# Kernel optimization log

Hardware: AMD Instinct MI355X
Metric: run time of the kernel (lower is better)

The kernel has to match this reference:

```python
import jax, jax.numpy as jnp
from jax import lax
import numpy as np

KS = 3
N = KS * KS
EPS = 1e-5


def conv2d(x, w, b=None, groups=1):
    out = lax.conv_general_dilated(x, w, (1, 1), 'SAME',
                                   feature_group_count=groups,
                                   dimension_numbers=('NCHW', 'OIHW', 'NCHW'))
    if b is not None:
        out = out + b[None, :, None, None]
    return out


def batchnorm(x, g, b):
    # training-mode BN (fresh nn.Module defaults to train): batch stats, biased var
    mu = x.mean((0, 2, 3), keepdims=True)
    var = ((x - mu) ** 2).mean((0, 2, 3), keepdims=True)
    return (x - mu) * lax.rsqrt(var + EPS) * g[None, :, None, None] + b[None, :, None, None]


def up2x_align_corners(x):
    # bilinear upsample, scale_factor=2, align_corners=True
    B, C, H, W = x.shape
    Ho, Wo = 2 * H, 2 * W

    def idx_w(n_in, n_out):
        c = jnp.arange(n_out, dtype=x.dtype) * ((n_in - 1) / (n_out - 1))
        i0 = jnp.clip(jnp.floor(c).astype(jnp.int32), 0, n_in - 2)
        t = c - i0.astype(x.dtype)
        return i0, t

    y0, ty = idx_w(H, Ho)
    x0, tx = idx_w(W, Wo)
    r = x[:, :, y0, :] * (1 - ty)[None, None, :, None] + x[:, :, y0 + 1, :] * ty[None, None, :, None]
    return r[:, :, :, x0] * (1 - tx) + r[:, :, :, x0 + 1] * tx


def gather_hw(xp, qx, qy):
    # xp: (B,C,Hp,Wp); qx,qy: (B,H,W,N) int -> (B,C,H,W,N)
    B, C, Hp, Wp = xp.shape
    flat = xp.reshape(B, C, Hp * Wp)
    idx = (qx * Wp + qy).reshape(B, 1, -1)
    idx = jnp.broadcast_to(idx, (B, C, idx.shape[-1]))
    return jnp.take_along_axis(flat, idx, axis=2).reshape(B, C, *qx.shape[1:])


def deform_conv(x, p_w, p_b, m_w, m_b, w):
    # modulated deformable conv v2 (4uiiurz1 impl), ks=3, stride=1, padding=1
    B, C, H, W = x.shape
    off = conv2d(x, p_w, p_b)                      # (B,2N,H,W)
    m = jax.nn.sigmoid(conv2d(x, m_w, m_b))        # (B,N,H,W)
    xp = jnp.pad(x, ((0, 0), (0, 0), (1, 1), (1, 1)))
    Hp, Wp = H + 2, W + 2
    off = jnp.transpose(off, (0, 2, 3, 1))         # (B,H,W,2N)
    pn_x = jnp.repeat(jnp.arange(-1, 2, dtype=x.dtype), KS)  # kernel row offsets, n=i*3+j
    pn_y = jnp.tile(jnp.arange(-1, 2, dtype=x.dtype), KS)
    p0_x = jnp.arange(1, H + 1, dtype=x.dtype)[None, :, None, None]
    p0_y = jnp.arange(1, W + 1, dtype=x.dtype)[None, None, :, None]
    px = p0_x + pn_x + off[..., :N]                # (B,H,W,N)
    py = p0_y + pn_y + off[..., N:]
    fx = jnp.floor(lax.stop_gradient(px))
    fy = jnp.floor(lax.stop_gradient(py))
    qx0 = jnp.clip(fx, 0, Hp - 1)
    qx1 = jnp.clip(fx + 1, 0, Hp - 1)
    qy0 = jnp.clip(fy, 0, Wp - 1)
    qy1 = jnp.clip(fy + 1, 0, Wp - 1)
    pxc = jnp.clip(px, 0, Hp - 1)
    pyc = jnp.clip(py, 0, Wp - 1)
    g_lt = (1 + (qx0 - pxc)) * (1 + (qy0 - pyc))
    g_rb = (1 - (qx1 - pxc)) * (1 - (qy1 - pyc))
    g_lb = (1 + (qx0 - pxc)) * (1 - (qy1 - pyc))
    g_rt = (1 - (qx1 - pxc)) * (1 + (qy0 - pyc))
    ix0, ix1 = qx0.astype(jnp.int32), qx1.astype(jnp.int32)
    iy0, iy1 = qy0.astype(jnp.int32), qy1.astype(jnp.int32)
    x_off = (g_lt[:, None] * gather_hw(xp, ix0, iy0)
             + g_rb[:, None] * gather_hw(xp, ix1, iy1)
             + g_lb[:, None] * gather_hw(xp, ix0, iy1)
             + g_rt[:, None] * gather_hw(xp, ix1, iy0))   # (B,C,H,W,N)
    x_off = x_off * jnp.transpose(m, (0, 2, 3, 1))[:, None]  # modulation
    O = w.shape[0]
    # equivalent to reshape to (B,C,H*ks,W*ks) then conv stride ks (bias=False)
    return jnp.einsum('bchwn,ocn->bohw', x_off, w.reshape(O, C, N))


def setup_inputs() -> dict:
    key = jax.random.key(0)
    ks = jax.random.split(key, 18)
    f = jnp.float32
    Cin, Cout = 256, 128
    inp = {
        'x1': jax.random.normal(ks[0], (8, 128, 32, 32), f),
        'x2': jax.random.normal(ks[1], (8, 128, 64, 64), f),
        'dsc_dw_w': jax.random.normal(ks[2], (Cin, 1, 3, 3), f) * 0.1,
        'dsc_dw_b': jax.random.normal(ks[3], (Cin,), f) * 0.05,
        'dsc_pw_w': jax.random.normal(ks[4], (Cout, Cin, 1, 1), f) * 0.05,
        'dsc_pw_b': jax.random.normal(ks[5], (Cout,), f) * 0.05,
        'p_w': jax.random.normal(ks[6], (2 * N, Cout, 3, 3), f) * 0.01,
        'p_b': jax.random.normal(ks[7], (2 * N,), f) * 0.01,
        'm_w': jax.random.normal(ks[8], (N, Cout, 3, 3), f) * 0.01,
        'm_b': jax.random.normal(ks[9], (N,), f) * 0.01,
        'dcn_w': jax.random.normal(ks[10], (Cout, Cout, 3, 3), f) * 0.05,
        'bn1_g': jnp.ones((Cout,), f),
        'bn1_b': jnp.zeros((Cout,), f),
        'dw2_w': jax.random.normal(ks[11], (Cout, 1, 3, 3), f) * 0.1,
        'dw2_b': jax.random.normal(ks[12], (Cout,), f) * 0.05,
        'bn2_g': jnp.ones((Cout,), f),
        'bn2_b': jnp.zeros((Cout,), f),
    }
    return inp


def reference(x1, x2, dsc_dw_w, dsc_dw_b, dsc_pw_w, dsc_pw_b, p_w, p_b, m_w, m_b,
              dcn_w, bn1_g, bn1_b, dw2_w, dw2_b, bn2_g, bn2_b):
    x1u = up2x_align_corners(x1)                 # (B,128,64,64); diffX=diffY=0 -> no pad
    x = jnp.concatenate([x2, x1u], axis=1)       # (B,256,64,64)
    h = conv2d(x, dsc_dw_w, dsc_dw_b, groups=x.shape[1])   # depthwise
    h = conv2d(h, dsc_pw_w, dsc_pw_b)                      # pointwise -> 128
    h = deform_conv(h, p_w, p_b, m_w, m_b, dcn_w)
    h = jax.nn.gelu(batchnorm(h, bn1_g, bn1_b), approximate=False)
    h = conv2d(h, dw2_w, dw2_b, groups=h.shape[1])         # depthwise k=3
    return jax.nn.relu(batchnorm(h, bn2_g, bn2_b))
```

## Files before the change

kernel.cpp:

```cpp
#include <hip/hip_runtime.h>
#include <math.h>

typedef const float* fp;
typedef __attribute__((ext_vector_type(8))) short short8;
typedef __attribute__((ext_vector_type(4))) float f32x4;

__device__ __forceinline__ unsigned short f2bf(float f){
    unsigned u = __float_as_uint(f);
    u += 0x7fff + ((u >> 16) & 1);
    return (unsigned short)(u >> 16);
}
__device__ __forceinline__ float bflo(unsigned u){ return __uint_as_float(u << 16); }
__device__ __forceinline__ float bfhi(unsigned u){ return __uint_as_float(u & 0xffff0000u); }
__device__ __forceinline__ unsigned cvtpk(float a, float b){
    unsigned r; asm("v_cvt_pk_bf16_f32 %0, %1, %2" : "=v"(r) : "v"(a), "v"(b)); return r;
}
__device__ __forceinline__ void st4bf(void* p, float a, float b, float c, float d){
    uint2 v; v.x = cvtpk(a,b); v.y = cvtpk(c,d);
    *(uint2*)p = v;
}

__global__ __launch_bounds__(256) void k_prep(fp dcn_w, fp pw, fp mw, fp pww,
                                              unsigned short* Wbf, unsigned short* Wpm,
                                              unsigned short* Wpwbf){
    int i = blockIdx.x*256 + threadIdx.x;
    if(i < 16384){
        int o = i >> 7, c = i & 127;
        const float* s = dcn_w + o*1152 + c*9;
        #pragma unroll
        for(int n=0;n<9;n++) Wbf[(n<<14) + (o<<7) + c] = f2bf(s[n]);
    } else if(i < 20480){
        int j = i - 16384;
        int q = j >> 7, c = j & 127;
        if(q < 18){
            const float* s = pw + q*1152 + c*9;
            #pragma unroll
            for(int n=0;n<9;n++) Wpm[(n<<12) + (q<<7) + c] = f2bf(s[n]);
        } else if(q < 27){
            const float* s = mw + (q-18)*1152 + c*9;
            #pragma unroll
            for(int n=0;n<9;n++) Wpm[(n<<12) + (q<<7) + c] = f2bf(s[n]);
        } else {
            #pragma unroll
            for(int n=0;n<9;n++) Wpm[(n<<12) + (q<<7) + c] = 0;
        }
    } else if(i < 53248){
        int j = i - 20480;
        Wpwbf[j] = f2bf(pww[j]);
    }
}

__global__ __launch_bounds__(256) void k_updw256(fp x1, fp x2, fp w, fp bias, unsigned short* Bo){
    __shared__ float sA[66*68 + 4];
    int bid = blockIdx.x;
    int c = bid & 255, b = bid >> 8;
    int tid = threadIdx.x;
    for(int j = tid; j < 264; j += 256){
        int idx;
        if(j < 66)       idx = j;
        else if(j < 132) idx = 65*68 + (j-66);
        else if(j < 196) idx = (j-132+1)*68;
        else if(j < 260) idx = (j-196+1)*68 + 65;
        else             idx = 66*68 + (j-260);
        sA[idx] = 0.f;
    }
    if(c < 128){
        const float* src = x2 + ((size_t)(b*128+c)<<12);
        for(int j = tid; j < 1024; j += 256){
            int yy = j >> 4, x4 = (j & 15) << 2;
            float4 v = *(const float4*)&src[(yy<<6) + x4];
            float* d = &sA[(yy+1)*68 + x4 + 1];
            d[0]=v.x; d[1]=v.y; d[2]=v.z; d[3]=v.w;
        }
    } else {
        int cc = c - 128;
        fp src = x1 + ((b*128+cc)<<10);
        const float s = 31.0f/63.0f;
        for(int j = tid; j < 4096; j += 256){
            int yy = j >> 6, xx = j & 63;
            float fy = yy*s, fx = xx*s;
            int iy = (int)fy; if (iy > 30) iy = 30;
            int ix = (int)fx; if (ix > 30) ix = 30;
            float ty = fy - (float)iy, tx = fx - (float)ix;
            float v00 = src[iy*32+ix],     v01 = src[iy*32+ix+1];
            float v10 = src[(iy+1)*32+ix], v11 = src[(iy+1)*32+ix+1];
            sA[(yy+1)*68 + xx + 1] =
                (v00*(1.f-ty)+v10*ty)*(1.f-tx) + (v01*(1.f-ty)+v11*ty)*tx;
        }
    }
    __syncthreads();
    float w0=w[c*9+0], w1=w[c*9+1], w2=w[c*9+2];
    float w3=w[c*9+3], w4=w[c*9+4], w5=w[c*9+5];
    float w6=w[c*9+6], w7=w[c*9+7], w8=w[c*9+8];
    float bv = bias[c];
    unsigned short* dst = Bo + ((size_t)(b*256+c)<<12);
    for(int j = tid; j < 1024; j += 256){
        int y = j >> 4, x0 = (j & 15) << 2;
        float a0=bv, a1=bv, a2=bv, a3=bv;
        #pragma unroll
        for(int ky=0; ky<3; ky++){
            const float* rr = &sA[(y+ky)*68 + x0];
            float4 u0 = *(const float4*)&rr[0];
            float2 u1 = *(const float2*)&rr[4];
            float wA = (ky==0)?w0:((ky==1)?w3:w6);
            float wB = (ky==0)?w1:((ky==1)?w4:w7);
            float wC = (ky==0)?w2:((ky==1)?w5:w8);
            a0 += wA*u0.x + wB*u0.y + wC*u0.z;
            a1 += wA*u0.y + wB*u0.z + wC*u0.w;
            a2 += wA*u0.z + wB*u0.w + wC*u1.x;
            a3 += wA*u0.w + wB*u1.x + wC*u1.y;
        }
        st4bf(&dst[(y<<6)+x0], a0,a1,a2,a3);
    }
}

#define PW_STAGE_X(kc, bufp) do{ \
    _Pragma("unroll") \
    for(int k_=0;k_<4;k_++){ \
        int j_ = tid + (k_<<9); \
        int cc_ = j_ >> 4, p4_ = (j_ & 15) << 2; \
        int c_ = ((kc)<<7) + cc_; \
        uint2 v_ = *(const uint2*)&Bo[((size_t)((b<<8)+c_)<<12) + pix0 + p4_]; \
        (bufp)[(p4_+0)*136 + cc_] = (unsigned short)(v_.x & 0xffffu); \
        (bufp)[(p4_+1)*136 + cc_] = (unsigned short)(v_.x >> 16); \
        (bufp)[(p4_+2)*136 + cc_] = (unsigned short)(v_.y & 0xffffu); \
        (bufp)[(p4_+3)*136 + cc_] = (unsigned short)(v_.y >> 16); \
    } }while(0)

#define PW_STAGE_W(kc) do{ \
    _Pragma("unroll") \
    for(int k_=0;k_<4;k_++){ \
        int j_ = tid + (k_<<9); \
        int o_ = j_ >> 4, cg_ = j_ & 15; \
        *(int4*)&sW[o_*136 + (cg_<<3)] = \
            *(const int4*)&Wpwbf[o_*256 + ((kc)<<7) + (cg_<<3)]; \
    } }while(0)

#define PW_DOMFMA(srcp) do{ \
    _Pragma("unroll") \
    for(int ks_=0; ks_<4; ks_++){ \
        int k0_ = ks_ << 5; \
        short8 bfr0 = *(const short8*)&(srcp)[(phb + m16)*136 + k0_ + (quad<<3)]; \
        short8 bfr1 = *(const short8*)&(srcp)[(phb + 16 + m16)*136 + k0_ + (quad<<3)]; \
        _Pragma("unroll") \
        for(int ot_=0;ot_<2;ot_++){ \
            short8 afr = *(const short8*)&sW[(wo + (ot_<<4) + m16)*136 + k0_ + (quad<<3)]; \
            acc[ot_][0] = __builtin_amdgcn_mfma_f32_16x16x32_bf16(afr, bfr0, acc[ot_][0], 0,0,0); \
            acc[ot_][1] = __builtin_amdgcn_mfma_f32_16x16x32_bf16(afr, bfr1, acc[ot_][1], 0,0,0); \
        } } }while(0)

__global__ __launch_bounds__(512, 2) void k_pw(const unsigned short* Bo, const unsigned short* Wpwbf,
                                               fp bias, unsigned short* Cbf){
    __shared__ __align__(16) unsigned short sW[128*136];
    __shared__ __align__(16) unsigned short sX[2][64*136];
    int b = blockIdx.x & 7;
    int pix0 = (blockIdx.x >> 3) << 6;
    int tid = threadIdx.x;
    int lane = tid & 63, wave = tid >> 6;
    int m16 = lane & 15, quad = lane >> 4;
    int wo  = (wave & 3) << 5;
    int phb = (wave >> 2) << 5;

    short8 ap = {0,0,0,0,0,0,0,0}, bpr = {0,0,0,0,0,0,0,0};
    if(quad == 0){
        ap[0]  = (short)f2bf((float)m16);
        bpr[0] = (short)f2bf((float)(m16+100));
    }
    f32x4 dp = {0.f,0.f,0.f,0.f};
    dp = __builtin_amdgcn_mfma_f32_16x16x32_bf16(ap, bpr, dp, 0,0,0);
    bool p1 = true;
    #pragma unroll
    for(int r=0;r<4;r++){
        float expP1 = (float)(quad*4+r) * (float)(m16+100);
        p1 = p1 && (fabsf(dp[r]-expP1) < 0.5f);
    }
    bool swapD = (__ballot(p1) != 0xFFFFFFFFFFFFFFFFull);

    f32x4 acc[2][2];
    #pragma unroll
    for(int i=0;i<2;i++){
        #pragma unroll
        for(int j=0;j<2;j++) acc[i][j] = (f32x4){0.f,0.f,0.f,0.f};
    }

    PW_STAGE_X(0, (&sX[0][0]));
    PW_STAGE_W(0);
    __syncthreads();
    PW_STAGE_X(1, (&sX[1][0]));
    PW_DOMFMA((&sX[0][0]));
    __syncthreads();
    PW_STAGE_W(1);
    __syncthreads();
    PW_DOMFMA((&sX[1][0]));

    if(!swapD){
        #pragma unroll
        for(int ot=0;ot<2;ot++){
            int o0 = wo + (ot<<4) + (quad<<2);
            float4 bv = *(const float4*)&bias[o0];
            #pragma unroll
            for(int pt=0;pt<2;pt++){
                int px = pix0 + phb + (pt<<4) + m16;
                st4bf(&Cbf[((size_t)((b<<12) + px))*128 + o0],
                      acc[ot][pt][0]+bv.x, acc[ot][pt][1]+bv.y,
                      acc[ot][pt][2]+bv.z, acc[ot][pt][3]+bv.w);
            }
        }
    } else {
        #pragma unroll
        for(int ot=0;ot<2;ot++){
            int o = wo + (ot<<4) + m16;
            float bv = bias[o];
            #pragma unroll
            for(int pt=0;pt<2;pt++){
                #pragma unroll
                for(int r=0;r<4;r++){
                    int px = pix0 + phb + (pt<<4) + (quad<<2) + r;
                    Cbf[((size_t)((b<<12) + px))*128 + o] = f2bf(acc[ot][pt][r] + bv);
                }
            }
        }
    }
}

__global__ __launch_bounds__(256, 2) void k_offmask(const unsigned short* Cbf, const unsigned short* Wpm,
                                                    fp pb, fp mb, float* OM){
    __shared__ __align__(16) unsigned short sWin[3*66*136];
    __shared__ __align__(16) unsigned short sW[2][32*136];
    int b = blockIdx.x & 7;
    int y = blockIdx.x >> 3;
    int pix0 = y << 6;
    int tid = threadIdx.x;
    int lane = tid & 63, wave = tid >> 6;
    int m16 = lane & 15, quad = lane >> 4;
    int wp = wave << 4;
    const unsigned short* cbf = Cbf + ((size_t)b<<12)*128;

    short8 ap = {0,0,0,0,0,0,0,0}, bpr = {0,0,0,0,0,0,0,0};
    if(quad == 0){
        ap[0]  = (short)f2bf((float)m16);
        bpr[0] = (short)f2bf((float)(m16+100));
    }
    f32x4 dp = {0.f,0.f,0.f,0.f};
    dp = __builtin_amdgcn_mfma_f32_16x16x32_bf16(ap, bpr, dp, 0,0,0);
    bool p1 = true;
    #pragma unroll
    for(int r=0;r<4;r++){
        float expP1 = (float)(quad*4+r) * (float)(m16+100);
        p1 = p1 && (fabsf(dp[r]-expP1) < 0.5f);
    }
    bool swapD = (__ballot(p1) != 0xFFFFFFFFFFFFFFFFull);

    f32x4 acc[2];
    acc[0] = (f32x4){0.f,0.f,0.f,0.f};
    acc[1] = (f32x4){0.f,0.f,0.f,0.f};

    {
        const int4* wsrc = (const int4*)Wpm;
        int4 wA_ = wsrc[tid], wB_ = wsrc[tid + 256];
        for(int i = tid; i < 3168; i += 256){
            int pos = i >> 4, g = i & 15;
            int r = pos / 66, col = pos - r*66;
            int yy = y + r - 1, xx = col - 1;
            int4 v = make_int4(0,0,0,0);
            if(yy>=0 && yy<64 && xx>=0 && xx<64)
                v = *(const int4*)&cbf[(size_t)((yy<<6)+xx)*128 + (g<<3)];
            *(int4*)&sWin[pos*136 + (g<<3)] = v;
        }
        *(int4*)&sW[0][(tid>>4)*136 + ((tid&15)<<3)] = wA_;
        int j = tid + 256;
        *(int4*)&sW[0][(j>>4)*136 + ((j&15)<<3)] = wB_;
    }
    __syncthreads();

    for(int n=0;n<9;n++){
        int4 wA_, wB_;
        if(n<8){
            const int4* wsrc = (const int4*)(Wpm + ((n+1)<<12));
            wA_ = wsrc[tid]; wB_ = wsrc[tid + 256];
        }
        int ky = n/3, kx = n - ky*3;
        const unsigned short* base = &sWin[(ky*66 + wp + kx)*136];
        #pragma unroll
        for(int ks=0; ks<4; ks++){
            int k0 = ks << 5;
            short8 bfr = *(const short8*)&base[m16*136 + k0 + (quad<<3)];
            #pragma unroll
            for(int qt=0;qt<2;qt++){
                short8 afr = *(const short8*)&sW[n&1][((qt<<4) + m16)*136 + k0 + (quad<<3)];
                acc[qt] = __builtin_amdgcn_mfma_f32_16x16x32_bf16(afr, bfr, acc[qt], 0,0,0);
            }
        }
        if(n<8){
            *(int4*)&sW[(n+1)&1][(tid>>4)*136 + ((tid&15)<<3)] = wA_;
            int j = tid + 256;
            *(int4*)&sW[(n+1)&1][(j>>4)*136 + ((j&15)<<3)] = wB_;
        }
        __syncthreads();
    }
    if(!swapD){
        #pragma unroll
        for(int qt=0;qt<2;qt++){
            int px = pix0 + wp + m16;
            #pragma unroll
            for(int r=0;r<4;r++){
                int q = (qt<<4) + (quad<<2) + r;
                if(q < 27){
                    float v = acc[qt][r] + ((q<18) ? pb[q] : mb[q-18]);
                    if(q>=18) v = 1.f/(1.f+expf(-v));
                    OM[((b*27+q)<<12) + px] = v;
                }
            }
        }
    } else {
        #pragma unroll
        for(int qt=0;qt<2;qt++){
            int q = (qt<<4) + m16;
            if(q < 27){
                float bias = (q<18) ? pb[q] : mb[q-18];
                #pragma unroll
                for(int r=0;r<4;r++){
                    int px = pix0 + wp + (quad<<2) + r;
                    float v = acc[qt][r] + bias;
                    if(q>=18) v = 1.f/(1.f+expf(-v));
                    OM[((b*27+q)<<12) + px] = v;
                }
            }
        }
    }
}

#define K5_META(t) do{ if(tid < 256){ \
    int px_ = tid >> 2, k_ = tid & 3; \
    int pix_ = pix0 + px_; \
    int yq_ = pix_ >> 6, xq_ = pix_ & 63; \
    int kyy_ = (t)/3, kxx_ = (t)-kyy_*3; \
    float oxv_ = omb[((t)<<12)+pix_]; \
    float oyv_ = omb[(((t)+9)<<12)+pix_]; \
    float mv_  = omb[(((t)+18)<<12)+pix_]; \
    float pxf_ = (float)(yq_ + kyy_) + oxv_; \
    float pyf_ = (float)(xq_ + kxx_) + oyv_; \
    float fx_ = floorf(pxf_), fy_ = floorf(pyf_); \
    float qx0_ = fminf(fmaxf(fx_,0.f),65.f),  qx1_ = fminf(fmaxf(fx_+1.f,0.f),65.f); \
    float qy0_ = fminf(fmaxf(fy_,0.f),65.f),  qy1_ = fminf(fmaxf(fy_+1.f,0.f),65.f); \
    float pxc_ = fminf(fmaxf(pxf_,0.f),65.f), pyc_ = fminf(fmaxf(pyf_,0.f),65.f); \
    float dx0_ = 1.f+(qx0_-pxc_), dx1_ = 1.f-(qx1_-pxc_); \
    float dy0_ = 1.f+(qy0_-pyc_), dy1_ = 1.f-(qy1_-pyc_); \
    int ax0_=(int)qx0_, ax1_=(int)qx1_, ay0_=(int)qy0_, ay1_=(int)qy1_; \
    bool vx0_ = (ax0_>=1)&&(ax0_<=64), vx1_ = (ax1_>=1)&&(ax1_<=64); \
    bool vy0_ = (ay0_>=1)&&(ay0_<=64), vy1_ = (ay1_>=1)&&(ay1_<=64); \
    int  axs_ = (k_&1) ? ax1_ : ax0_; \
    int  ays_ = (k_==1||k_==2) ? ay1_ : ay0_; \
    bool vxs_ = (k_&1) ? vx1_ : vx0_; \
    bool vys_ = (k_==1||k_==2) ? vy1_ : vy0_; \
    float dxs_ = (k_&1) ? dx1_ : dx0_; \
    float dys_ = (k_==1||k_==2) ? dy1_ : dy0_; \
    bool v_ = vxs_ && vys_; \
    int base_ = v_ ? (((axs_-1)<<6)+(ays_-1)) : 0; \
    float g_ = v_ ? dxs_*dys_*mv_ : 0.f; \
    sM[tid] = make_uint2((unsigned)base_, __float_as_uint(g_)); \
} }while(0)

#define K5_GATHER(bufp) do{ \
    _Pragma("unroll") \
    for(int j_=0;j_<4;j_++){ \
        int px_ = pxb + (j_<<4); \
        uint2 e0_ = sM[(px_<<2)+0]; \
        uint2 e1_ = sM[(px_<<2)+1]; \
        uint2 e2_ = sM[(px_<<2)+2]; \
        uint2 e3_ = sM[(px_<<2)+3]; \
        float g0_ = __uint_as_float(e0_.y), g1_ = __uint_as_float(e1_.y); \
        float g2_ = __uint_as_float(e2_.y), g3_ = __uint_as_float(e3_.y); \
        uint2 c0_ = *(const uint2*)&cb[((size_t)e0_.x<<7) + cg4]; \
        uint2 c1_ = *(const uint2*)&cb[((size_t)e1_.x<<7) + cg4]; \
        uint2 c2_ = *(const uint2*)&cb[((size_t)e2_.x<<7) + cg4]; \
        uint2 c3_ = *(const uint2*)&cb[((size_t)e3_.x<<7) + cg4]; \
        float vx_ = g0_*bflo(c0_.x) + g1_*bflo(c1_.x) + g2_*bflo(c2_.x) + g3_*bflo(c3_.x); \
        float vy_ = g0_*bfhi(c0_.x) + g1_*bfhi(c1_.x) + g2_*bfhi(c2_.x) + g3_*bfhi(c3_.x); \
        float vz_ = g0_*bflo(c0_.y) + g1_*bflo(c1_.y) + g2_*bflo(c2_.y) + g3_*bflo(c3_.y); \
        float vw_ = g0_*bfhi(c0_.y) + g1_*bfhi(c1_.y) + g2_*bfhi(c2_.y) + g3_*bfhi(c3_.y); \
        st4bf(&(bufp)[px_*136 + cg4], vx_, vy_, vz_, vw_); \
    } }while(0)

#define K5_STAGE_W(t) do{ \
    const int4* wsrc_ = (const int4*)(Wbf + ((t)<<14)); \
    _Pragma("unroll") \
    for(int k_=0;k_<4;k_++){ int j_ = tid + (k_<<9); \
        *(int4*)&sW[(j_>>4)*136 + ((j_&15)<<3)] = wsrc_[j_]; } }while(0)

#define K5_DOMFMA(srcp) do{ \
    _Pragma("unroll") \
    for(int ks_=0; ks_<4; ks_++){ \
        int k0_ = ks_ << 5; \
        short8 bfr0 = *(const short8*)&(srcp)[(phb + m16)*136 + k0_ + (quad<<3)]; \
        short8 bfr1 = *(const short8*)&(srcp)[(phb + 16 + m16)*136 + k0_ + (quad<<3)]; \
        _Pragma("unroll") \
        for(int ot_=0;ot_<2;ot_++){ \
            short8 afr = *(const short8*)&sW[(wo + (ot_<<4) + m16)*136 + k0_ + (quad<<3)]; \
            acc[ot_][0] = __builtin_amdgcn_mfma_f32_16x16x32_bf16(afr, bfr0, acc[ot_][0], 0,0,0); \
            acc[ot_][1] = __builtin_amdgcn_mfma_f32_16x16x32_bf16(afr, bfr1, acc[ot_][1], 0,0,0); \
        } } }while(0)

__global__ __launch_bounds__(512, 2) void k_deform(const unsigned short* Cbf, fp OM,
                                                   const unsigned short* Wbf,
                                                   unsigned short* D, float* stats){
    __shared__ __align__(16) unsigned short sW[128*136];
    __shared__ __align__(16) unsigned short sX[2][64*136];
    __shared__ __align__(8)  uint2 sM[256];
    int b = blockIdx.x & 7;
    int pix0 = (blockIdx.x >> 3) << 6;
    int tid = threadIdx.x;
    int lane = tid & 63, wave = tid >> 6;
    int m16 = lane & 15, quad = lane >> 4;
    int wo  = (wave & 3) << 5;
    int phb = (wave >> 2) << 5;
    int cg4 = (tid & 31) << 2;
    int pxb = tid >> 5;
    const float* omb = OM + b*27*4096;
    const unsigned short* cb = Cbf + ((size_t)b<<12)*128;

    short8 ap = {0,0,0,0,0,0,0,0}, bpr = {0,0,0,0,0,0,0,0};
    if(quad == 0){
        ap[0]  = (short)f2bf((float)m16);
        bpr[0] = (short)f2bf((float)(m16+100));
    }
    f32x4 dp = {0.f,0.f,0.f,0.f};
    dp = __builtin_amdgcn_mfma_f32_16x16x32_bf16(ap, bpr, dp, 0,0,0);
    bool p1 = true;
    #pragma unroll
    for(int r=0;r<4;r++){
        float expP1 = (float)(quad*4+r) * (float)(m16+100);
        p1 = p1 && (fabsf(dp[r]-expP1) < 0.5f);
    }
    bool swapD = (__ballot(p1) != 0xFFFFFFFFFFFFFFFFull);

    f32x4 acc[2][2];
    #pragma unroll
    for(int i=0;i<2;i++){
        #pragma unroll
        for(int j=0;j<2;j++) acc[i][j] = (f32x4){0.f,0.f,0.f,0.f};
    }

    K5_META(0);
    __syncthreads();
    K5_GATHER((&sX[0][0]));
    K5_STAGE_W(0);
    __syncthreads();
    K5_META(1);
    __syncthreads();

    for(int n=0;n<9;n++){
        if(n<8) K5_GATHER((&sX[(n+1)&1][0]));
        K5_DOMFMA((&sX[n&1][0]));
        __syncthreads();
        if(n<8){
            K5_STAGE_W(n+1);
            if(n<7) K5_META(n+2);
            __syncthreads();
        }
    }

    float* sdq = (float*)&sX[0][0];
    if(tid < 256) sdq[tid] = 0.f;
    __syncthreads();
    if(!swapD){
        #pragma unroll
        for(int ot=0;ot<2;ot++){
            #pragma unroll
            for(int pt=0;pt<2;pt++){
                int px = pix0 + phb + (pt<<4) + m16;
                #pragma unroll
                for(int r=0;r<4;r++){
                    int o = wo + (ot<<4) + (quad<<2) + r;
                    D[((size_t)(b*128+o)<<12) + px] = f2bf(acc[ot][pt][r]);
                }
            }
        }
        #pragma unroll
        for(int ot=0;ot<2;ot++){
            #pragma unroll
            for(int r=0;r<4;r++){
                float s  = acc[ot][0][r] + acc[ot][1][r];
                float s2 = acc[ot][0][r]*acc[ot][0][r] + acc[ot][1][r]*acc[ot][1][r];
                #pragma unroll
                for(int msk=1; msk<16; msk<<=1){
                    s  += __shfl_xor(s, msk, 64);
                    s2 += __shfl_xor(s2, msk, 64);
                }
                if(m16 == 0){
                    int o = wo + (ot<<4) + (quad<<2) + r;
                    atomicAdd(&sdq[o], s);
                    atomicAdd(&sdq[128+o], s2);
                }
            }
        }
    } else {
        #pragma unroll
        for(int ot=0;ot<2;ot++){
            #pragma unroll
            for(int pt=0;pt<2;pt++){
                int o = wo + (ot<<4) + m16;
                #pragma unroll
                for(int r=0;r<4;r++){
                    int px = pix0 + phb + (pt<<4) + (quad<<2) + r;
                    D[((size_t)(b*128+o)<<12) + px] = f2bf(acc[ot][pt][r]);
                }
            }
        }
        #pragma unroll
        for(int ot=0;ot<2;ot++){
            float s = 0.f, s2 = 0.f;
            #pragma unroll
            for(int pt=0;pt<2;pt++){
                #pragma unroll
                for(int r=0;r<4;r++){
                    float v = acc[ot][pt][r];
                    s += v; s2 += v*v;
                }
            }
            #pragma unroll
            for(int msk=16; msk<64; msk<<=1){
                s  += __shfl_xor(s, msk, 64);
                s2 += __shfl_xor(s2, msk, 64);
            }
            if(quad == 0){
                int o = wo + (ot<<4) + m16;
                atomicAdd(&sdq[o], s);
                atomicAdd(&sdq[128+o], s2);
            }
        }
    }
    __syncthreads();
    if(tid < 128){
        atomicAdd(&stats[tid],     sdq[tid]);
        atomicAdd(&stats[128+tid], sdq[128+tid]);
    }
}

__global__ __launch_bounds__(256) void k_bngelu_dw128(const unsigned short* Dsrc, float* stats,
                                                      fp g1, fp b1, fp w, fp bias, unsigned short* Hs){
    __shared__ float sG[66*68 + 4];
    __shared__ float sd[256], sq[256];
    int bid = blockIdx.x;
    int c = bid & 127, b = bid >> 7;
    int tid = threadIdx.x;
    float mean1 = stats[c] * (1.f/32768.f);
    float var1  = stats[128+c] * (1.f/32768.f) - mean1*mean1;
    float rstd1 = rsqrtf(var1 + 1e-5f);
    float sc = rstd1 * g1[c];
    float sb = b1[c] - mean1*sc;
    for(int j = tid; j < 264; j += 256){
        int idx;
        if(j < 66)       idx = j;
        else if(j < 132) idx = 65*68 + (j-66);
        else if(j < 196) idx = (j-132+1)*68;
        else if(j < 260) idx = (j-196+1)*68 + 65;
        else             idx = 66*68 + (j-260);
        sG[idx] = 0.f;
    }
    const unsigned short* dplane = Dsrc + ((size_t)(b*128+c)<<12);
    for(int j = tid; j < 1024; j += 256){
        int yy = j >> 4, x4 = (j & 15) << 2;
        uint2 v = *(const uint2*)&dplane[(yy<<6) + x4];
        float g0 = bflo(v.x)*sc+sb, g1v = bfhi(v.x)*sc+sb;
        float g2 = bflo(v.y)*sc+sb, g3 = bfhi(v.y)*sc+sb;
        float* d = &sG[(yy+1)*68 + x4 + 1];
        d[0] = 0.5f*g0*(1.0f + erff(g0*0.70710678118654752f));
        d[1] = 0.5f*g1v*(1.0f + erff(g1v*0.70710678118654752f));
        d[2] = 0.5f*g2*(1.0f + erff(g2*0.70710678118654752f));
        d[3] = 0.5f*g3*(1.0f + erff(g3*0.70710678118654752f));
    }
    __syncthreads();
    float w0=w[c*9+0], w1=w[c*9+1], w2=w[c*9+2];
    float w3=w[c*9+3], w4=w[c*9+4], w5=w[c*9+5];
    float w6=w[c*9+6], w7=w[c*9+7], w8=w[c*9+8];
    float bv = bias[c];
    unsigned short* dst = Hs + ((size_t)(b*128+c)<<12);
    float s = 0.f, s2 = 0.f;
    for(int j = tid; j < 1024; j += 256){
        int y = j >> 4, x0 = (j & 15) << 2;
        float a0=bv, a1=bv, a2=bv, a3=bv;
        #pragma unroll
        for(int ky=0; ky<3; ky++){
            const float* rr = &sG[(y+ky)*68 + x0];
            float4 u0 = *(const float4*)&rr[0];
            float2 u1 = *(const float2*)&rr[4];
            float wA = (ky==0)?w0:((ky==1)?w3:w6);
            float wB = (ky==0)?w1:((ky==1)?w4:w7);
            float wC = (ky==0)?w2:((ky==1)?w5:w8);
            a0 += wA*u0.x + wB*u0.y + wC*u0.z;
            a1 += wA*u0.y + wB*u0.z + wC*u0.w;
            a2 += wA*u0.z + wB*u0.w + wC*u1.x;
            a3 += wA*u0.w + wB*u1.x + wC*u1.y;
        }
        st4bf(&dst[(y<<6)+x0], a0,a1,a2,a3);
        s += a0+a1+a2+a3;
        s2 += a0*a0 + a1*a1 + a2*a2 + a3*a3;
    }
    sd[tid]=s; sq[tid]=s2; __syncthreads();
    for(int off=128; off>0; off>>=1){
        if(tid<off){ sd[tid]+=sd[tid+off]; sq[tid]+=sq[tid+off]; }
        __syncthreads();
    }
    if(tid==0){
        atomicAdd(&stats[256+c], sd[0]);
        atomicAdd(&stats[384+c], sq[0]);
    }
}

__global__ __launch_bounds__(256) void k_bn_relu_out(const unsigned short* Hs, const float* stats,
                                                     fp g, fp bb, float* out){
    int idx = blockIdx.x*256+threadIdx.x;
    int c = (idx>>10)&127;
    float mean2 = stats[256+c] * (1.f/32768.f);
    float var2  = stats[384+c] * (1.f/32768.f) - mean2*mean2;
    float rs = rsqrtf(var2 + 1e-5f) * g[c];
    float sb = bb[c] - mean2*rs;
    uint2 v = ((const uint2*)Hs)[idx];
    float4 o;
    o.x = fmaxf(bflo(v.x)*rs+sb, 0.f);
    o.y = fmaxf(bfhi(v.x)*rs+sb, 0.f);
    o.z = fmaxf(bflo(v.y)*rs+sb, 0.f);
    o.w = fmaxf(bfhi(v.y)*rs+sb, 0.f);
    ((float4*)out)[idx] = o;
}

extern "C" void kernel_launch(void* const* d_in, const int* in_sizes, int n_in,
                              void* d_out, int out_size, void* d_ws, size_t ws_size,
                              hipStream_t stream){
    fp x1   = (fp)d_in[0];
    fp x2   = (fp)d_in[1];
    fp dw_w = (fp)d_in[2];  fp dw_b = (fp)d_in[3];
    fp pw_w = (fp)d_in[4];  fp pw_b = (fp)d_in[5];
    fp p_w  = (fp)d_in[6];  fp p_b  = (fp)d_in[7];
    fp m_w  = (fp)d_in[8];  fp m_b  = (fp)d_in[9];
    fp dcn_w= (fp)d_in[10];
    fp bn1g = (fp)d_in[11]; fp bn1b = (fp)d_in[12];
    fp dw2w = (fp)d_in[13]; fp dw2b = (fp)d_in[14];
    fp bn2g = (fp)d_in[15]; fp bn2b = (fp)d_in[16];

    float* ws  = (float*)d_ws;
    unsigned short* Bo  = (unsigned short*)ws;
    unsigned short* Cbf = (unsigned short*)(ws + 8388608);
    unsigned short* Hs  = (unsigned short*)(ws + 8388608);
    float* OM  = ws + 12582912;
    unsigned short* Wbf = (unsigned short*)(ws + 13467648);
    unsigned short* Wpm = (unsigned short*)(ws + 13541376);
    float* stats = ws + 13559808;
    unsigned short* Wpwbf = (unsigned short*)(ws + 13560320);
    unsigned short* D   = Bo;
    float* out = (float*)d_out;

    hipMemsetAsync(stats, 0, 512*sizeof(float), stream);
    k_prep         <<<208,   256, 0, stream>>>(dcn_w, p_w, m_w, pw_w, Wbf, Wpm, Wpwbf);
    k_updw256      <<<2048,  256, 0, stream>>>(x1, x2, dw_w, dw_b, Bo);
    k_pw           <<<512,   512, 0, stream>>>(Bo, Wpwbf, pw_b, Cbf);
    k_offmask      <<<512,   256, 0, stream>>>(Cbf, Wpm, p_b, m_b, OM);
    k_deform       <<<512,   512, 0, stream>>>(Cbf, OM, Wbf, D, stats);
    k_bngelu_dw128 <<<1024,  256, 0, stream>>>(D, stats, bn1g, bn1b, dw2w, dw2b, Hs);
    k_bn_relu_out  <<<4096,  256, 0, stream>>>(Hs, stats, bn2g, bn2b, out);
}
```

Baseline: 196.1 us.

## Fuse offset/mask conv into deformable conv kernel via shared-memory staging

The separate offset/mask convolution kernel is removed. Its MFMA computation now runs at the start of k_deform, writing the 27 offset/mask channels for the block's row into shared memory instead of a global OM buffer. The LDS is unioned so the input window and weight buffers are reused for the later deform stages. This removes one launch and the global round-trip for OM, but it adds a prologue with extra syncs to each deform block and may change occupancy through the LDS footprint.

```diff
diff --git a/kernel.cpp b/kernel.cpp
--- a/kernel.cpp
+++ b/kernel.cpp
@@ -223,121 +223,13 @@
     }
 }
 
-__global__ __launch_bounds__(256, 2) void k_offmask(const unsigned short* Cbf, const unsigned short* Wpm,
-                                                    fp pb, fp mb, float* OM){
-    __shared__ __align__(16) unsigned short sWin[3*66*136];
-    __shared__ __align__(16) unsigned short sW[2][32*136];
-    int b = blockIdx.x & 7;
-    int y = blockIdx.x >> 3;
-    int pix0 = y << 6;
-    int tid = threadIdx.x;
-    int lane = tid & 63, wave = tid >> 6;
-    int m16 = lane & 15, quad = lane >> 4;
-    int wp = wave << 4;
-    const unsigned short* cbf = Cbf + ((size_t)b<<12)*128;
-
-    short8 ap = {0,0,0,0,0,0,0,0}, bpr = {0,0,0,0,0,0,0,0};
-    if(quad == 0){
-        ap[0]  = (short)f2bf((float)m16);
-        bpr[0] = (short)f2bf((float)(m16+100));
-    }
-    f32x4 dp = {0.f,0.f,0.f,0.f};
-    dp = __builtin_amdgcn_mfma_f32_16x16x32_bf16(ap, bpr, dp, 0,0,0);
-    bool p1 = true;
-    #pragma unroll
-    for(int r=0;r<4;r++){
-        float expP1 = (float)(quad*4+r) * (float)(m16+100);
-        p1 = p1 && (fabsf(dp[r]-expP1) < 0.5f);
-    }
-    bool swapD = (__ballot(p1) != 0xFFFFFFFFFFFFFFFFull);
-
-    f32x4 acc[2];
-    acc[0] = (f32x4){0.f,0.f,0.f,0.f};
-    acc[1] = (f32x4){0.f,0.f,0.f,0.f};
-
-    {
-        const int4* wsrc = (const int4*)Wpm;
-        int4 wA_ = wsrc[tid], wB_ = wsrc[tid + 256];
-        for(int i = tid; i < 3168; i += 256){
-            int pos = i >> 4, g = i & 15;
-            int r = pos / 66, col = pos - r*66;
-            int yy = y + r - 1, xx = col - 1;
-            int4 v = make_int4(0,0,0,0);
-            if(yy>=0 && yy<64 && xx>=0 && xx<64)
-                v = *(const int4*)&cbf[(size_t)((yy<<6)+xx)*128 + (g<<3)];
-            *(int4*)&sWin[pos*136 + (g<<3)] = v;
-        }
-        *(int4*)&sW[0][(tid>>4)*136 + ((tid&15)<<3)] = wA_;
-        int j = tid + 256;
-        *(int4*)&sW[0][(j>>4)*136 + ((j&15)<<3)] = wB_;
-    }
-    __syncthreads();
-
-    for(int n=0;n<9;n++){
-        int4 wA_, wB_;
-        if(n<8){
-            const int4* wsrc = (const int4*)(Wpm + ((n+1)<<12));
-            wA_ = wsrc[tid]; wB_ = wsrc[tid + 256];
-        }
-        int ky = n/3, kx = n - ky*3;
-        const unsigned short* base = &sWin[(ky*66 + wp + kx)*136];
-        #pragma unroll
-        for(int ks=0; ks<4; ks++){
-            int k0 = ks << 5;
-            short8 bfr = *(const short8*)&base[m16*136 + k0 + (quad<<3)];
-            #pragma unroll
-            for(int qt=0;qt<2;qt++){
-                short8 afr = *(const short8*)&sW[n&1][((qt<<4) + m16)*136 + k0 + (quad<<3)];
-                acc[qt] = __builtin_amdgcn_mfma_f32_16x16x32_bf16(afr, bfr, acc[qt], 0,0,0);
-            }
-        }
-        if(n<8){
-            *(int4*)&sW[(n+1)&1][(tid>>4)*136 + ((tid&15)<<3)] = wA_;
-            int j = tid + 256;
-            *(int4*)&sW[(n+1)&1][(j>>4)*136 + ((j&15)<<3)] = wB_;
-        }
-        __syncthreads();
-    }
-    if(!swapD){
-        #pragma unroll
-        for(int qt=0;qt<2;qt++){
-            int px = pix0 + wp + m16;
-            #pragma unroll
-            for(int r=0;r<4;r++){
-                int q = (qt<<4) + (quad<<2) + r;
-                if(q < 27){
-                    float v = acc[qt][r] + ((q<18) ? pb[q] : mb[q-18]);
-                    if(q>=18) v = 1.f/(1.f+expf(-v));
-                    OM[((b*27+q)<<12) + px] = v;
-                }
-            }
-        }
-    } else {
-        #pragma unroll
-        for(int qt=0;qt<2;qt++){
-            int q = (qt<<4) + m16;
-            if(q < 27){
-                float bias = (q<18) ? pb[q] : mb[q-18];
-                #pragma unroll
-                for(int r=0;r<4;r++){
-                    int px = pix0 + wp + (quad<<2) + r;
-                    float v = acc[qt][r] + bias;
-                    if(q>=18) v = 1.f/(1.f+expf(-v));
-                    OM[((b*27+q)<<12) + px] = v;
-                }
-            }
-        }
-    }
-}
-
 #define K5_META(t) do{ if(tid < 256){ \
     int px_ = tid >> 2, k_ = tid & 3; \
-    int pix_ = pix0 + px_; \
-    int yq_ = pix_ >> 6, xq_ = pix_ & 63; \
+    int yq_ = y, xq_ = px_; \
     int kyy_ = (t)/3, kxx_ = (t)-kyy_*3; \
-    float oxv_ = omb[((t)<<12)+pix_]; \
-    float oyv_ = omb[(((t)+9)<<12)+pix_]; \
-    float mv_  = omb[(((t)+18)<<12)+pix_]; \
+    float oxv_ = sOM[((t)<<6)+px_]; \
+    float oyv_ = sOM[(((t)+9)<<6)+px_]; \
+    float mv_  = sOM[(((t)+18)<<6)+px_]; \
     float pxf_ = (float)(yq_ + kyy_) + oxv_; \
     float pyf_ = (float)(xq_ + kxx_) + oyv_; \
     float fx_ = floorf(pxf_), fy_ = floorf(pyf_); \
@@ -401,14 +293,15 @@
             acc[ot_][1] = __builtin_amdgcn_mfma_f32_16x16x32_bf16(afr, bfr1, acc[ot_][1], 0,0,0); \
         } } }while(0)
 
-__global__ __launch_bounds__(512, 2) void k_deform(const unsigned short* Cbf, fp OM,
+__global__ __launch_bounds__(512, 2) void k_deform(const unsigned short* Cbf,
+                                                   const unsigned short* Wpm, fp pb, fp mb,
                                                    const unsigned short* Wbf,
                                                    unsigned short* D, float* stats){
-    __shared__ __align__(16) unsigned short sW[128*136];
-    __shared__ __align__(16) unsigned short sX[2][64*136];
-    __shared__ __align__(8)  uint2 sM[256];
+    __shared__ __align__(16) unsigned short uLDS[35840];
+    __shared__ __align__(16) float sOM[27*64];
     int b = blockIdx.x & 7;
-    int pix0 = (blockIdx.x >> 3) << 6;
+    int y = blockIdx.x >> 3;
+    int pix0 = y << 6;
     int tid = threadIdx.x;
     int lane = tid & 63, wave = tid >> 6;
     int m16 = lane & 15, quad = lane >> 4;
@@ -416,7 +309,6 @@
     int phb = (wave >> 2) << 5;
     int cg4 = (tid & 31) << 2;
     int pxb = tid >> 5;
-    const float* omb = OM + b*27*4096;
     const unsigned short* cb = Cbf + ((size_t)b<<12)*128;
 
     short8 ap = {0,0,0,0,0,0,0,0}, bpr = {0,0,0,0,0,0,0,0};
@@ -434,6 +326,75 @@
     }
     bool swapD = (__ballot(p1) != 0xFFFFFFFFFFFFFFFFull);
 
+    {
+        unsigned short* sWin  = uLDS;
+        unsigned short* sWpm0 = uLDS + 26928;
+        unsigned short* sWpm1 = uLDS + 31024;
+        int qt = wave & 1, pt = wave >> 1;
+        int4 w0_ = ((const int4*)Wpm)[tid];
+        for(int i = tid; i < 3168; i += 512){
+            int pos = i >> 4, g = i & 15;
+            int r = pos / 66, col = pos - r*66;
+            int yy = y + r - 1, xx = col - 1;
+            int4 v = make_int4(0,0,0,0);
+            if(yy>=0 && yy<64 && xx>=0 && xx<64)
+                v = *(const int4*)&cb[(size_t)((yy<<6)+xx)*128 + (g<<3)];
+            *(int4*)&sWin[pos*136 + (g<<3)] = v;
+        }
+        *(int4*)&sWpm0[(tid>>4)*136 + ((tid&15)<<3)] = w0_;
+        __syncthreads();
+
+        f32x4 accA = {0.f,0.f,0.f,0.f};
+        for(int n=0;n<9;n++){
+            int4 wn_;
+            if(n<8) wn_ = ((const int4*)(Wpm + ((n+1)<<12)))[tid];
+            int ky = n/3, kx = n - ky*3;
+            const unsigned short* base = &sWin[(ky*66 + (pt<<4) + kx)*136];
+            const unsigned short* swp = (n&1) ? sWpm1 : sWpm0;
+            #pragma unroll
+            for(int ks=0; ks<4; ks++){
+                int k0 = ks << 5;
+                short8 bfr = *(const short8*)&base[m16*136 + k0 + (quad<<3)];
+                short8 afr = *(const short8*)&swp[((qt<<4) + m16)*136 + k0 + (quad<<3)];
+                accA = __builtin_amdgcn_mfma_f32_16x16x32_bf16(afr, bfr, accA, 0,0,0);
+            }
+            if(n<8){
+                unsigned short* swn = ((n+1)&1) ? sWpm1 : sWpm0;
+                *(int4*)&swn[(tid>>4)*136 + ((tid&15)<<3)] = wn_;
+            }
+            __syncthreads();
+        }
+        if(!swapD){
+            int pxl = (pt<<4) + m16;
+            #pragma unroll
+            for(int r=0;r<4;r++){
+                int q = (qt<<4) + (quad<<2) + r;
+                if(q < 27){
+                    float v = accA[r] + ((q<18) ? pb[q] : mb[q-18]);
+                    if(q>=18) v = 1.f/(1.f+expf(-v));
+                    sOM[(q<<6) + pxl] = v;
+                }
+            }
+        } else {
+            int q = (qt<<4) + m16;
+            if(q < 27){
+                float bias2 = (q<18) ? pb[q] : mb[q-18];
+                #pragma unroll
+                for(int r=0;r<4;r++){
+                    int pxl = (pt<<4) + (quad<<2) + r;
+                    float v = accA[r] + bias2;
+                    if(q>=18) v = 1.f/(1.f+expf(-v));
+                    sOM[(q<<6) + pxl] = v;
+                }
+            }
+        }
+        __syncthreads();
+    }
+
+    unsigned short* sW = uLDS;
+    unsigned short* sXb = uLDS + 17408;
+    uint2* sM = (uint2*)(uLDS + 34816);
+
     f32x4 acc[2][2];
     #pragma unroll
     for(int i=0;i<2;i++){
@@ -443,15 +404,15 @@
 
     K5_META(0);
     __syncthreads();
-    K5_GATHER((&sX[0][0]));
+    K5_GATHER((sXb));
     K5_STAGE_W(0);
     __syncthreads();
     K5_META(1);
     __syncthreads();
 
     for(int n=0;n<9;n++){
-        if(n<8) K5_GATHER((&sX[(n+1)&1][0]));
-        K5_DOMFMA((&sX[n&1][0]));
+        if(n<8) K5_GATHER((sXb + (((n+1)&1)*8704)));
+        K5_DOMFMA((sXb + ((n&1)*8704)));
         __syncthreads();
         if(n<8){
             K5_STAGE_W(n+1);
@@ -460,7 +421,7 @@
         }
     }
 
-    float* sdq = (float*)&sX[0][0];
+    float* sdq = (float*)uLDS;
     if(tid < 256) sdq[tid] = 0.f;
     __syncthreads();
     if(!swapD){
@@ -643,7 +604,6 @@
     unsigned short* Bo  = (unsigned short*)ws;
     unsigned short* Cbf = (unsigned short*)(ws + 8388608);
     unsigned short* Hs  = (unsigned short*)(ws + 8388608);
-    float* OM  = ws + 12582912;
     unsigned short* Wbf = (unsigned short*)(ws + 13467648);
     unsigned short* Wpm = (unsigned short*)(ws + 13541376);
     float* stats = ws + 13559808;
@@ -655,8 +615,7 @@
     k_prep         <<<208,   256, 0, stream>>>(dcn_w, p_w, m_w, pw_w, Wbf, Wpm, Wpwbf);
     k_updw256      <<<2048,  256, 0, stream>>>(x1, x2, dw_w, dw_b, Bo);
     k_pw           <<<512,   512, 0, stream>>>(Bo, Wpwbf, pw_b, Cbf);
-    k_offmask      <<<512,   256, 0, stream>>>(Cbf, Wpm, p_b, m_b, OM);
-    k_deform       <<<512,   512, 0, stream>>>(Cbf, OM, Wbf, D, stats);
+    k_deform       <<<512,   512, 0, stream>>>(Cbf, Wpm, p_b, m_b, Wbf, D, stats);
     k_bngelu_dw128 <<<1024,  256, 0, stream>>>(D, stats, bn1g, bn1b, dw2w, dw2b, Hs);
     k_bn_relu_out  <<<4096,  256, 0, stream>>>(Hs, stats, bn2g, bn2b, out);
 }
```

Result: no change. 194.8 us (-0.7%).
